# Performance work log

Hardware: AMD Instinct MI355X
Metric: run time of the kernel (lower is better)

The kernel has to match this reference:

```python
import jax, jax.numpy as jnp
import numpy as np

H = 128   # hidden_size
DYN = 2   # dynamic_features


def setup_inputs() -> dict:
    B, S, STAT = 256, 64, 2
    key = jax.random.key(0)
    ks = jax.random.split(key, 9)
    sc = 0.05
    return {
        "static": jax.random.normal(ks[0], (B, STAT, S), jnp.float32),
        "static_embeddings": jax.random.normal(ks[1], (B, H, S), jnp.float32),
        "dynamic": jax.random.uniform(ks[2], (B, DYN, S), jnp.float32),
        # dynamic_embedding: Conv1d(2 -> 128, k=1)
        "dyn_w": jax.random.normal(ks[3], (H, DYN), jnp.float32) * sc,
        "dyn_b": jnp.zeros((H,), jnp.float32),
        # decoder_input_dynamic_embedding: Conv1d(128 -> 128, k=1)
        "in_w": jax.random.normal(ks[4], (H, H), jnp.float32) * sc,
        "in_b": jnp.zeros((H,), jnp.float32),
        # GRU (single layer, batch_first), torch gate order r,z,n
        "w_ih": jax.random.normal(ks[5], (3 * H, H), jnp.float32) * sc,
        "w_hh": jax.random.normal(ks[6], (3 * H, H), jnp.float32) * sc,
        "b_ih": jnp.zeros((3 * H,), jnp.float32),
        "b_hh": jnp.zeros((3 * H,), jnp.float32),
        # DoubleAttention: scores = v . tanh(W [static; dynamic; hidden])
        "W_att": jax.random.normal(ks[7], (H, 3 * H), jnp.float32) * sc,
        "v_att": jax.random.normal(ks[8], (H,), jnp.float32) * sc,
    }


def _pointer_forward(static_embeddings, dynamic, dyn_w, dyn_b, in_w, in_b,
                     w_ih, w_hh, b_ih, b_hh, W_att, v_att):
    B, Hd, S = static_embeddings.shape
    NEG = jnp.asarray(-1e9, static_embeddings.dtype)
    base = jax.random.key(42)

    def gru_cell(x, h):  # torch nn.GRU single step
        gi = x @ w_ih.T + b_ih
        gh = h @ w_hh.T + b_hh
        ir, iz, i_n = jnp.split(gi, 3, axis=-1)
        hr, hz, h_n = jnp.split(gh, 3, axis=-1)
        r = jax.nn.sigmoid(ir + hr)
        z = jax.nn.sigmoid(iz + hz)
        n = jnp.tanh(i_n + r * h_n)
        return (1.0 - z) * n + z * h

    first_mask = jnp.zeros((B, S), static_embeddings.dtype).at[:, 0].set(1.0)

    def step(carry, i):
        dec_in, h, visited, dyn = carry
        # decoder_input_dynamic_embedding: 1x1 conv == per-token linear
        x = dec_in @ in_w.T + in_b                      # [B,H]
        h = gru_cell(x, h)                              # decoder_output == new hidden
        # i==0: only depot (index 0) is selectable; afterwards: unvisited nodes
        mask = jnp.where(i == 0, first_mask, 1.0 - visited)
        dyn_emb = jnp.einsum('bds,hd->bhs', dyn, dyn_w) + dyn_b[None, :, None]
        ctx = jnp.concatenate(
            [static_embeddings, dyn_emb,
             jnp.broadcast_to(h[:, :, None], (B, Hd, S))], axis=1)  # [B,3H,S]
        scores = jnp.einsum('h,bhs->bs', v_att,
                            jnp.tanh(jnp.einsum('hk,bks->bhs', W_att, ctx)))
        logits = jnp.where(mask > 0, scores, NEG)       # -inf on masked positions
        ptr = jax.random.categorical(jax.random.fold_in(base, i), logits)  # sample
        logp = jnp.take_along_axis(jax.nn.log_softmax(logits, -1),
                                   ptr[:, None], axis=1)[:, 0]
        sel = (jnp.arange(S)[None, :] == ptr[:, None]).astype(dyn.dtype)  # [B,S]
        visited = jnp.maximum(visited, sel)
        dyn = dyn * (1.0 - sel)[:, None, :]             # update_dynamic_state
        # original feeds the (conv-transformed) decoder input back to itself
        return (x, h, visited, dyn), (ptr, logp)

    init = (static_embeddings[:, :, 0],                  # decoder_input = emb of node 0
            jnp.zeros((B, Hd), static_embeddings.dtype),  # GRU hidden
            jnp.zeros((B, S), static_embeddings.dtype),   # visited
            dynamic)
    _, (tours, logps) = jax.lax.scan(step, init, jnp.arange(S))
    return tours.T, logps.T  # [B,S], [B,S]


def reference(static, static_embeddings, dynamic, dyn_w, dyn_b, in_w, in_b,
              w_ih, w_hh, b_ih, b_hh, W_att, v_att):
    # dropout layers are identity in eval mode; `static` is only used for logging
    return _pointer_forward(static_embeddings, dynamic, dyn_w, dyn_b, in_w, in_b,
                            w_ih, w_hh, b_ih, b_hh, W_att, v_att)
```

## Files before the change

kernel.cpp:

```cpp
#include <hip/hip_runtime.h>
#include <stdint.h>


#define BN 256
#define SN 64
#define HN 128
#define NEGV (-1.0e9f)
#define TINYF 1.17549435e-38f

#define OFF_A   0
#define OFF_GI  8192
#define OFF_WHC 8192
#define OFF_SET 16384
#define OFF_UT  24832
#define OFF_HC  33280
#define OFF_KK  33536
#define OFF_SV  33664
#define OFF_DY  33792
#define OFF_WD  33920
#define OFF_CV  34176
#define SMEM_FLOATS 34304

__device__ __forceinline__ uint32_t rotl32(uint32_t v, int d) {
  return (v << d) | (v >> (32 - d));
}

__device__ __forceinline__ void threefry2x32(uint32_t k0, uint32_t k1,
                                             uint32_t x0, uint32_t x1,
                                             uint32_t& o0, uint32_t& o1) {
  uint32_t ks2 = k0 ^ k1 ^ 0x1BD11BDAu;
  x0 += k0; x1 += k1;
  x0 += x1; x1 = rotl32(x1, 13); x1 ^= x0;
  x0 += x1; x1 = rotl32(x1, 15); x1 ^= x0;
  x0 += x1; x1 = rotl32(x1, 26); x1 ^= x0;
  x0 += x1; x1 = rotl32(x1, 6);  x1 ^= x0;
  x0 += k1; x1 += ks2 + 1u;
  x0 += x1; x1 = rotl32(x1, 17); x1 ^= x0;
  x0 += x1; x1 = rotl32(x1, 29); x1 ^= x0;
  x0 += x1; x1 = rotl32(x1, 16); x1 ^= x0;
  x0 += x1; x1 = rotl32(x1, 24); x1 ^= x0;
  x0 += ks2; x1 += k0 + 2u;
  x0 += x1; x1 = rotl32(x1, 13); x1 ^= x0;
  x0 += x1; x1 = rotl32(x1, 15); x1 ^= x0;
  x0 += x1; x1 = rotl32(x1, 26); x1 ^= x0;
  x0 += x1; x1 = rotl32(x1, 6);  x1 ^= x0;
  x0 += k0; x1 += k1 + 3u;
  x0 += x1; x1 = rotl32(x1, 17); x1 ^= x0;
  x0 += x1; x1 = rotl32(x1, 29); x1 ^= x0;
  x0 += x1; x1 = rotl32(x1, 16); x1 ^= x0;
  x0 += x1; x1 = rotl32(x1, 24); x1 ^= x0;
  x0 += k1; x1 += ks2 + 4u;
  x0 += x1; x1 = rotl32(x1, 13); x1 ^= x0;
  x0 += x1; x1 = rotl32(x1, 15); x1 ^= x0;
  x0 += x1; x1 = rotl32(x1, 26); x1 ^= x0;
  x0 += x1; x1 = rotl32(x1, 6);  x1 ^= x0;
  x0 += ks2; x1 += k0 + 5u;
  o0 = x0; o1 = x1;
}

__device__ __forceinline__ float jax_gumbel(uint32_t k0, uint32_t k1, int j) {
  uint32_t o0, o1;
  threefry2x32(k0, k1, 0u, (uint32_t)j, o0, o1);
  uint32_t bits = o0 ^ o1;
  uint32_t ub = (bits >> 9) | 0x3F800000u;
  float u = __uint_as_float(ub) - 1.0f;
  u = fmaxf(u + TINYF, TINYF);
  return -logf(-logf(u));
}

__device__ __forceinline__ float ftanh(float x) {
  float ax = fabsf(x);
  float e = __expf(-2.0f * ax);
  float r = (1.0f - e) * __builtin_amdgcn_rcpf(1.0f + e);
  return copysignf(r, x);
}

__device__ __forceinline__ float fsig(float x) {
  return __builtin_amdgcn_rcpf(1.0f + __expf(-x));
}

__global__ void k0_dyn(const float* __restrict__ W_att, const float* __restrict__ dyn_w,
                       const float* __restrict__ dyn_b, float* __restrict__ Wd,
                       float* __restrict__ cv) {
  int h = threadIdx.x;
  float w0 = 0.f, w1 = 0.f, cc = 0.f;
  for (int k = 0; k < HN; ++k) {
    float w = W_att[h * 384 + 128 + k];
    w0 = fmaf(w, dyn_w[2 * k + 0], w0);
    w1 = fmaf(w, dyn_w[2 * k + 1], w1);
    cc = fmaf(w, dyn_b[k], cc);
  }
  Wd[2 * h] = w0; Wd[2 * h + 1] = w1; cv[h] = cc;
}

__global__ __launch_bounds__(1024) void mega(
    const float* __restrict__ SE, const float* __restrict__ dynamic,
    const float* __restrict__ in_w, const float* __restrict__ in_b,
    const float* __restrict__ w_ih, const float* __restrict__ b_ih,
    const float* __restrict__ w_hh, const float* __restrict__ b_hh,
    const float* __restrict__ W_att, const float* __restrict__ v_att,
    const float* __restrict__ Wd, const float* __restrict__ cv,
    float* __restrict__ out) {
  extern __shared__ float sm[];
  int b = blockIdx.x, t = threadIdx.x;
  float* A   = sm + OFF_A;
  float* GIl = sm + OFF_GI;
  float* WHC = sm + OFF_WHC;
  float* SET = sm + OFF_SET;
  float* UT  = sm + OFF_UT;
  float* HC  = sm + OFF_HC;
  uint32_t* KK = (uint32_t*)(sm + OFF_KK);
  float* SV  = sm + OFF_SV;
  float* DY  = sm + OFF_DY;
  float* WDs = sm + OFF_WD;
  float* CVs = sm + OFF_CV;

  int ml = t >> 3, ks = t & 7;

  if (t < 64) {
    uint32_t o0, o1;
    threefry2x32(0u, 42u, 0u, (uint32_t)t, o0, o1);
    KK[2 * t] = o0; KK[2 * t + 1] = o1;
  }
  if (t < 128) {
    SV[t]  = v_att[t];
    DY[t]  = dynamic[b * 128 + t];
    CVs[t] = cv[t];
    HC[t]  = SE[b * 8192 + t * 64];
  }
  if (t < 256) WDs[t] = Wd[t];
  __syncthreads();

  {
    float4 wv[4];
#pragma unroll
    for (int q = 0; q < 4; ++q)
      wv[q] = *(const float4*)(in_w + ml * HN + q * 32 + ks * 4);
    float bib = in_b[ml];
    for (int ii = 0; ii < SN; ++ii) {
      const float* xc = HC + (ii & 1) * 128;
      float* xn = HC + ((ii + 1) & 1) * 128;
      float a0 = 0.f, a1 = 0.f, a2 = 0.f, a3 = 0.f;
#pragma unroll
      for (int q = 0; q < 4; ++q) {
        float4 x4 = *(const float4*)(xc + q * 32 + ks * 4);
        a0 = fmaf(wv[q].x, x4.x, a0);
        a1 = fmaf(wv[q].y, x4.y, a1);
        a2 = fmaf(wv[q].z, x4.z, a2);
        a3 = fmaf(wv[q].w, x4.w, a3);
      }
      float s = (a0 + a1) + (a2 + a3);
      s += __shfl_xor(s, 1); s += __shfl_xor(s, 2); s += __shfl_xor(s, 4);
      if (ks == 0) {
        float xv = s + bib;
        A[ii * 128 + ml] = xv;
        xn[ml] = xv;
      }
      __syncthreads();
    }
  }

  {
    float4 wv[3][4]; float bi[3];
#pragma unroll
    for (int j = 0; j < 3; ++j) {
#pragma unroll
      for (int q = 0; q < 4; ++q)
        wv[j][q] = *(const float4*)(w_ih + (ml + 128 * j) * HN + q * 32 + ks * 4);
      bi[j] = b_ih[ml + 128 * j];
    }
    for (int n = 0; n < SN; ++n) {
      float4 x4[4];
#pragma unroll
      for (int q = 0; q < 4; ++q)
        x4[q] = *(const float4*)(A + n * 128 + q * 32 + ks * 4);
      float sum[3];
#pragma unroll
      for (int j = 0; j < 3; ++j) {
        float a0 = 0.f, a1 = 0.f, a2 = 0.f, a3 = 0.f;
#pragma unroll
        for (int q = 0; q < 4; ++q) {
          a0 = fmaf(wv[j][q].x, x4[q].x, a0);
          a1 = fmaf(wv[j][q].y, x4[q].y, a1);
          a2 = fmaf(wv[j][q].z, x4[q].z, a2);
          a3 = fmaf(wv[j][q].w, x4[q].w, a3);
        }
        float s = (a0 + a1) + (a2 + a3);
        s += __shfl_xor(s, 1); s += __shfl_xor(s, 2); s += __shfl_xor(s, 4);
        sum[j] = s + bi[j];
      }
      if (ks == 0) {
#pragma unroll
        for (int j = 0; j < 3; ++j) GIl[n * 384 + ml + 128 * j] = sum[j];
      }
    }
    __syncthreads();
  }

  if (t < 256) HC[t] = 0.f;
  __syncthreads();
  {
    float4 wv[3][4]; float bh[3];
#pragma unroll
    for (int j = 0; j < 3; ++j) {
#pragma unroll
      for (int q = 0; q < 4; ++q)
        wv[j][q] = *(const float4*)(w_hh + (ml + 128 * j) * HN + q * 32 + ks * 4);
      bh[j] = b_hh[ml + 128 * j];
    }
    float hp = 0.f;
    for (int ii = 0; ii < SN; ++ii) {
      const float* hcr = HC + (ii & 1) * 128;
      float* hcw = HC + ((ii + 1) & 1) * 128;
      float4 x4[4];
#pragma unroll
      for (int q = 0; q < 4; ++q)
        x4[q] = *(const float4*)(hcr + q * 32 + ks * 4);
      float sum[3];
#pragma unroll
      for (int j = 0; j < 3; ++j) {
        float a0 = 0.f, a1 = 0.f, a2 = 0.f, a3 = 0.f;
#pragma unroll
        for (int q = 0; q < 4; ++q) {
          a0 = fmaf(wv[j][q].x, x4[q].x, a0);
          a1 = fmaf(wv[j][q].y, x4[q].y, a1);
          a2 = fmaf(wv[j][q].z, x4[q].z, a2);
          a3 = fmaf(wv[j][q].w, x4[q].w, a3);
        }
        float s = (a0 + a1) + (a2 + a3);
        s += __shfl_xor(s, 1); s += __shfl_xor(s, 2); s += __shfl_xor(s, 4);
        sum[j] = s + bh[j];
      }
      if (ks == 0) {
        const float* gr = GIl + ii * 384;
        float r = fsig(gr[ml] + sum[0]);
        float z = fsig(gr[128 + ml] + sum[1]);
        float nn = ftanh(gr[256 + ml] + r * sum[2]);
        float hn = (1.0f - z) * nn + z * hp;
        hcw[ml] = hn;
        A[ii * 128 + ml] = hn;
        hp = hn;
      }
      __syncthreads();
    }
  }

  {
    float4 wv[4];
#pragma unroll
    for (int q = 0; q < 4; ++q)
      wv[q] = *(const float4*)(W_att + ml * 384 + 256 + q * 32 + ks * 4);
    for (int n = 0; n < SN; ++n) {
      float a0 = 0.f, a1 = 0.f, a2 = 0.f, a3 = 0.f;
#pragma unroll
      for (int q = 0; q < 4; ++q) {
        float4 x4 = *(const float4*)(A + n * 128 + q * 32 + ks * 4);
        a0 = fmaf(wv[q].x, x4.x, a0);
        a1 = fmaf(wv[q].y, x4.y, a1);
        a2 = fmaf(wv[q].z, x4.z, a2);
        a3 = fmaf(wv[q].w, x4.w, a3);
      }
      float s = (a0 + a1) + (a2 + a3);
      s += __shfl_xor(s, 1); s += __shfl_xor(s, 2); s += __shfl_xor(s, 4);
      if (ks == 0) WHC[n * 128 + ml] = s;
    }
    __syncthreads();
  }

#pragma unroll
  for (int p = 0; p < 8; ++p) {
    int idx = p * 1024 + t;
    int h = idx >> 6, s = idx & 63;
    SET[s * 132 + h] = SE[b * 8192 + idx];
  }
  __syncthreads();

  {
    float4 wv[4];
#pragma unroll
    for (int q = 0; q < 4; ++q)
      wv[q] = *(const float4*)(W_att + ml * 384 + q * 32 + ks * 4);
    float wd0 = WDs[2 * ml], wd1 = WDs[2 * ml + 1], cvm = CVs[ml];
    for (int n = 0; n < SN; ++n) {
      float a0 = 0.f, a1 = 0.f, a2 = 0.f, a3 = 0.f;
#pragma unroll
      for (int q = 0; q < 4; ++q) {
        float4 x4 = *(const float4*)(SET + n * 132 + q * 32 + ks * 4);
        a0 = fmaf(wv[q].x, x4.x, a0);
        a1 = fmaf(wv[q].y, x4.y, a1);
        a2 = fmaf(wv[q].z, x4.z, a2);
        a3 = fmaf(wv[q].w, x4.w, a3);
      }
      float s = (a0 + a1) + (a2 + a3);
      s += __shfl_xor(s, 1); s += __shfl_xor(s, 2); s += __shfl_xor(s, 4);
      if (ks == 0) {
        float d0 = DY[n], d1 = DY[64 + n];
        UT[ml * 66 + n] = s + wd0 * d0 + wd1 * d1 + cvm;
      }
    }
    __syncthreads();
  }

  {
    int s = t & 63, w = t >> 6;
    float acc[4];
#pragma unroll
    for (int j = 0; j < 4; ++j) acc[j] = 0.f;
    for (int h = 0; h < HN; h += 4) {
      float u0 = UT[(h + 0) * 66 + s];
      float u1 = UT[(h + 1) * 66 + s];
      float u2 = UT[(h + 2) * 66 + s];
      float u3 = UT[(h + 3) * 66 + s];
      float4 v4 = *(const float4*)(SV + h);
#pragma unroll
      for (int j = 0; j < 4; ++j) {
        float4 wh = *(const float4*)(WHC + (w * 4 + j) * 128 + h);
        float a = acc[j];
        a = fmaf(v4.x, ftanh(u0 + wh.x), a);
        a = fmaf(v4.y, ftanh(u1 + wh.y), a);
        a = fmaf(v4.z, ftanh(u2 + wh.z), a);
        a = fmaf(v4.w, ftanh(u3 + wh.w), a);
        acc[j] = a;
      }
    }
    __syncthreads();
#pragma unroll
    for (int j = 0; j < 4; ++j) A[(w * 4 + j) * 64 + s] = acc[j];
    __syncthreads();
  }

  {
    float* G = A + 4096;
#pragma unroll
    for (int p = 0; p < 4; ++p) {
      int idx = p * 1024 + t;
      int i = idx >> 6;
      G[idx] = jax_gumbel(KK[2 * i], KK[2 * i + 1], b * 64 + (idx & 63));
    }
    __syncthreads();
  }

  if (t < 64) {
    const float* Pl = A;
    const float* Gl = A + 4096;
    int s = t;
    bool visited = false;
    for (int i = 0; i < SN; ++i) {
      float score = Pl[i * 64 + s];
      bool allowed = (i == 0) ? (s == 0) : (!visited);
      float logit = allowed ? score : NEGV;
      float z = logit + Gl[i * 64 + s];
      float bz = z; int bi = s;
#pragma unroll
      for (int off = 32; off > 0; off >>= 1) {
        float oz = __shfl_xor(bz, off);
        int oi = __shfl_xor(bi, off);
        if (oz > bz || (oz == bz && oi < bi)) { bz = oz; bi = oi; }
      }
      int ptr = bi;
      float m = logit;
#pragma unroll
      for (int off = 32; off > 0; off >>= 1) m = fmaxf(m, __shfl_xor(m, off));
      float e = expf(logit - m);
      float sum = e;
#pragma unroll
      for (int off = 32; off > 0; off >>= 1) sum += __shfl_xor(sum, off);
      float chosen = __shfl(logit, ptr);
      float logp = (chosen - m) - logf(sum);
      if (s == ptr) visited = true;
      if (s == 0) {
        out[b * SN + i] = (float)ptr;
        out[BN * SN + b * SN + i] = logp;
      }
    }
  }
}

extern "C" void kernel_launch(void* const* d_in, const int* in_sizes, int n_in,
                              void* d_out, int out_size, void* d_ws, size_t ws_size,
                              hipStream_t stream) {
  const float* SE    = (const float*)d_in[1];
  const float* dynam = (const float*)d_in[2];
  const float* dyn_w = (const float*)d_in[3];
  const float* dyn_b = (const float*)d_in[4];
  const float* in_w  = (const float*)d_in[5];
  const float* in_b  = (const float*)d_in[6];
  const float* w_ih  = (const float*)d_in[7];
  const float* w_hh  = (const float*)d_in[8];
  const float* b_ih  = (const float*)d_in[9];
  const float* b_hh  = (const float*)d_in[10];
  const float* W_att = (const float*)d_in[11];
  const float* v_att = (const float*)d_in[12];
  float* out = (float*)d_out;
  float* ws = (float*)d_ws;

  float* Wd = ws;
  float* cv = ws + 256;

  (void)hipFuncSetAttribute((const void*)mega,
                            hipFuncAttributeMaxDynamicSharedMemorySize,
                            SMEM_FLOATS * 4);

  hipLaunchKernelGGL(k0_dyn, dim3(1), dim3(128), 0, stream,
                     W_att, dyn_w, dyn_b, Wd, cv);
  hipLaunchKernelGGL(mega, dim3(BN), dim3(1024), SMEM_FLOATS * 4, stream,
                     SE, dynam, in_w, in_b, w_ih, b_ih, w_hh, b_hh,
                     W_att, v_att, Wd, cv, out);
}
```

Measured before the change: 347.3 us.

## Split mega kernel into recurrence and attention kernels with 512-thread blocks

The single 1024-thread-per-batch kernel becomes two 512-thread kernels. The first runs the input-embedding recurrence, the register-blocked GI projection (written to global scratch) and the GRU recurrence, with w_hh split between LDS and registers and GI prefetched two steps ahead. The second does the attention projections, scoring, Gumbel sampling and pointer selection, reading hidden states back from global memory. Threefry key generation moves to the setup kernel. The change aims to cut per-step sync cost in the sequential recurrences and raise occupancy, at the price of extra global traffic and a second launch.

```diff
diff --git a/kernel.cpp b/kernel.cpp
--- a/kernel.cpp
+++ b/kernel.cpp
@@ -7,19 +7,6 @@
 #define HN 128
 #define NEGV (-1.0e9f)
 #define TINYF 1.17549435e-38f
-
-#define OFF_A   0
-#define OFF_GI  8192
-#define OFF_WHC 8192
-#define OFF_SET 16384
-#define OFF_UT  24832
-#define OFF_HC  33280
-#define OFF_KK  33536
-#define OFF_SV  33664
-#define OFF_DY  33792
-#define OFF_WD  33920
-#define OFF_CV  34176
-#define SMEM_FLOATS 34304
 
 __device__ __forceinline__ uint32_t rotl32(uint32_t v, int d) {
   return (v << d) | (v >> (32 - d));
@@ -81,8 +68,13 @@
 
 __global__ void k0_dyn(const float* __restrict__ W_att, const float* __restrict__ dyn_w,
                        const float* __restrict__ dyn_b, float* __restrict__ Wd,
-                       float* __restrict__ cv) {
+                       float* __restrict__ cv, uint32_t* __restrict__ keys) {
   int h = threadIdx.x;
+  if (h < 64) {
+    uint32_t o0, o1;
+    threefry2x32(0u, 42u, 0u, (uint32_t)h, o0, o1);
+    keys[2 * h] = o0; keys[2 * h + 1] = o1;
+  }
   float w0 = 0.f, w1 = 0.f, cc = 0.f;
   for (int k = 0; k < HN; ++k) {
     float w = W_att[h * 384 + 128 + k];
@@ -93,64 +85,49 @@
   Wd[2 * h] = w0; Wd[2 * h + 1] = w1; cv[h] = cc;
 }
 
-__global__ __launch_bounds__(1024) void mega(
-    const float* __restrict__ SE, const float* __restrict__ dynamic,
+#define AB_A   0
+#define AB_WL  8192
+#define AB_HC  34304
+#define AB_GSH 34560
+#define AB_SMEM (34944 * 4)
+
+__global__ __launch_bounds__(512) void kAB(
+    const float* __restrict__ SE,
     const float* __restrict__ in_w, const float* __restrict__ in_b,
     const float* __restrict__ w_ih, const float* __restrict__ b_ih,
     const float* __restrict__ w_hh, const float* __restrict__ b_hh,
-    const float* __restrict__ W_att, const float* __restrict__ v_att,
-    const float* __restrict__ Wd, const float* __restrict__ cv,
-    float* __restrict__ out) {
+    float* __restrict__ GI_g, float* __restrict__ H_g) {
   extern __shared__ float sm[];
+  float* A   = sm + AB_A;
+  float* WL  = sm + AB_WL;
+  float* HC  = sm + AB_HC;
+  float* GSH = sm + AB_GSH;
   int b = blockIdx.x, t = threadIdx.x;
-  float* A   = sm + OFF_A;
-  float* GIl = sm + OFF_GI;
-  float* WHC = sm + OFF_WHC;
-  float* SET = sm + OFF_SET;
-  float* UT  = sm + OFF_UT;
-  float* HC  = sm + OFF_HC;
-  uint32_t* KK = (uint32_t*)(sm + OFF_KK);
-  float* SV  = sm + OFF_SV;
-  float* DY  = sm + OFF_DY;
-  float* WDs = sm + OFF_WD;
-  float* CVs = sm + OFF_CV;
-
-  int ml = t >> 3, ks = t & 7;
-
-  if (t < 64) {
-    uint32_t o0, o1;
-    threefry2x32(0u, 42u, 0u, (uint32_t)t, o0, o1);
-    KK[2 * t] = o0; KK[2 * t + 1] = o1;
-  }
-  if (t < 128) {
-    SV[t]  = v_att[t];
-    DY[t]  = dynamic[b * 128 + t];
-    CVs[t] = cv[t];
-    HC[t]  = SE[b * 8192 + t * 64];
-  }
-  if (t < 256) WDs[t] = Wd[t];
+
+  if (t < 128) HC[t] = SE[b * 8192 + t * 64];
   __syncthreads();
 
   {
-    float4 wv[4];
-#pragma unroll
-    for (int q = 0; q < 4; ++q)
-      wv[q] = *(const float4*)(in_w + ml * HN + q * 32 + ks * 4);
+    int ml = t >> 2, ks = t & 3;
+    float4 wv[8];
+#pragma unroll
+    for (int q = 0; q < 8; ++q)
+      wv[q] = *(const float4*)(in_w + ml * HN + q * 16 + ks * 4);
     float bib = in_b[ml];
     for (int ii = 0; ii < SN; ++ii) {
       const float* xc = HC + (ii & 1) * 128;
       float* xn = HC + ((ii + 1) & 1) * 128;
       float a0 = 0.f, a1 = 0.f, a2 = 0.f, a3 = 0.f;
 #pragma unroll
-      for (int q = 0; q < 4; ++q) {
-        float4 x4 = *(const float4*)(xc + q * 32 + ks * 4);
+      for (int q = 0; q < 8; ++q) {
+        float4 x4 = *(const float4*)(xc + q * 16 + ks * 4);
         a0 = fmaf(wv[q].x, x4.x, a0);
         a1 = fmaf(wv[q].y, x4.y, a1);
         a2 = fmaf(wv[q].z, x4.z, a2);
         a3 = fmaf(wv[q].w, x4.w, a3);
       }
       float s = (a0 + a1) + (a2 + a3);
-      s += __shfl_xor(s, 1); s += __shfl_xor(s, 2); s += __shfl_xor(s, 4);
+      s += __shfl_xor(s, 1); s += __shfl_xor(s, 2);
       if (ks == 0) {
         float xv = s + bib;
         A[ii * 128 + ml] = xv;
@@ -160,141 +137,198 @@
     }
   }
 
-  {
-    float4 wv[3][4]; float bi[3];
-#pragma unroll
-    for (int j = 0; j < 3; ++j) {
-#pragma unroll
-      for (int q = 0; q < 4; ++q)
-        wv[j][q] = *(const float4*)(w_ih + (ml + 128 * j) * HN + q * 32 + ks * 4);
-      bi[j] = b_ih[ml + 128 * j];
-    }
-    for (int n = 0; n < SN; ++n) {
-      float4 x4[4];
-#pragma unroll
-      for (int q = 0; q < 4; ++q)
-        x4[q] = *(const float4*)(A + n * 128 + q * 32 + ks * 4);
-      float sum[3];
-#pragma unroll
-      for (int j = 0; j < 3; ++j) {
-        float a0 = 0.f, a1 = 0.f, a2 = 0.f, a3 = 0.f;
-#pragma unroll
-        for (int q = 0; q < 4; ++q) {
-          a0 = fmaf(wv[j][q].x, x4[q].x, a0);
-          a1 = fmaf(wv[j][q].y, x4[q].y, a1);
-          a2 = fmaf(wv[j][q].z, x4[q].z, a2);
-          a3 = fmaf(wv[j][q].w, x4[q].w, a3);
+  for (int idx = t; idx < 24576; idx += 512) {
+    int m = idx >> 6, k = idx & 63;
+    WL[m * 68 + k] = w_hh[m * 128 + k];
+  }
+
+  {
+    int ml = t >> 2, ks = t & 3;
+    float bi[3];
+#pragma unroll
+    for (int j = 0; j < 3; ++j) bi[j] = b_ih[ml + 128 * j];
+    for (int g = 0; g < 8; ++g) {
+      float acc[3][8];
+#pragma unroll
+      for (int j = 0; j < 3; ++j)
+#pragma unroll
+        for (int nn = 0; nn < 8; ++nn) acc[j][nn] = 0.f;
+#pragma unroll
+      for (int p = 0; p < 4; ++p) {
+        float4 wv[3][2];
+#pragma unroll
+        for (int j = 0; j < 3; ++j) {
+          wv[j][0] = *(const float4*)(w_ih + (ml + 128 * j) * HN + p * 32 + ks * 4);
+          wv[j][1] = *(const float4*)(w_ih + (ml + 128 * j) * HN + p * 32 + 16 + ks * 4);
         }
-        float s = (a0 + a1) + (a2 + a3);
-        s += __shfl_xor(s, 1); s += __shfl_xor(s, 2); s += __shfl_xor(s, 4);
-        sum[j] = s + bi[j];
-      }
-      if (ks == 0) {
-#pragma unroll
-        for (int j = 0; j < 3; ++j) GIl[n * 384 + ml + 128 * j] = sum[j];
-      }
-    }
-    __syncthreads();
-  }
-
+#pragma unroll
+        for (int nn = 0; nn < 8; ++nn) {
+          int n = g * 8 + nn;
+          float4 x0 = *(const float4*)(A + n * 128 + p * 32 + ks * 4);
+          float4 x1 = *(const float4*)(A + n * 128 + p * 32 + 16 + ks * 4);
+#pragma unroll
+          for (int j = 0; j < 3; ++j) {
+            float a = acc[j][nn];
+            a = fmaf(wv[j][0].x, x0.x, a);
+            a = fmaf(wv[j][0].y, x0.y, a);
+            a = fmaf(wv[j][0].z, x0.z, a);
+            a = fmaf(wv[j][0].w, x0.w, a);
+            a = fmaf(wv[j][1].x, x1.x, a);
+            a = fmaf(wv[j][1].y, x1.y, a);
+            a = fmaf(wv[j][1].z, x1.z, a);
+            a = fmaf(wv[j][1].w, x1.w, a);
+            acc[j][nn] = a;
+          }
+        }
+      }
+#pragma unroll
+      for (int j = 0; j < 3; ++j)
+#pragma unroll
+        for (int nn = 0; nn < 8; ++nn) {
+          float s = acc[j][nn];
+          s += __shfl_xor(s, 1); s += __shfl_xor(s, 2);
+          if (ks == 0)
+            GI_g[b * 24576 + (g * 8 + nn) * 384 + ml + 128 * j] = s + bi[j];
+        }
+    }
+  }
+  __threadfence();
   if (t < 256) HC[t] = 0.f;
   __syncthreads();
-  {
-    float4 wv[3][4]; float bh[3];
+
+  {
+    int ml = t >> 2, ks = t & 3;
+    const float4* WL4 = (const float4*)WL;
+    float4 wu[3][4]; float bh[3];
 #pragma unroll
     for (int j = 0; j < 3; ++j) {
 #pragma unroll
       for (int q = 0; q < 4; ++q)
-        wv[j][q] = *(const float4*)(w_hh + (ml + 128 * j) * HN + q * 32 + ks * 4);
+        wu[j][q] = *(const float4*)(w_hh + (ml + 128 * j) * HN + 64 + q * 16 + ks * 4);
       bh[j] = b_hh[ml + 128 * j];
+    }
+    float gv0 = 0.f, gv1 = 0.f;
+    if (t < 384) {
+      gv0 = GI_g[b * 24576 + 0 * 384 + t];
+      gv1 = GI_g[b * 24576 + 1 * 384 + t];
     }
     float hp = 0.f;
     for (int ii = 0; ii < SN; ++ii) {
       const float* hcr = HC + (ii & 1) * 128;
       float* hcw = HC + ((ii + 1) & 1) * 128;
-      float4 x4[4];
-#pragma unroll
-      for (int q = 0; q < 4; ++q)
-        x4[q] = *(const float4*)(hcr + q * 32 + ks * 4);
-      float sum[3];
-#pragma unroll
-      for (int j = 0; j < 3; ++j) {
-        float a0 = 0.f, a1 = 0.f, a2 = 0.f, a3 = 0.f;
-#pragma unroll
-        for (int q = 0; q < 4; ++q) {
-          a0 = fmaf(wv[j][q].x, x4[q].x, a0);
-          a1 = fmaf(wv[j][q].y, x4[q].y, a1);
-          a2 = fmaf(wv[j][q].z, x4[q].z, a2);
-          a3 = fmaf(wv[j][q].w, x4[q].w, a3);
-        }
-        float s = (a0 + a1) + (a2 + a3);
-        s += __shfl_xor(s, 1); s += __shfl_xor(s, 2); s += __shfl_xor(s, 4);
-        sum[j] = s + bh[j];
-      }
+      float s0 = 0.f, s1 = 0.f, s2 = 0.f;
+#pragma unroll
+      for (int q = 0; q < 4; ++q) {
+        float4 xl = *(const float4*)(hcr + q * 16 + ks * 4);
+        float4 xu = *(const float4*)(hcr + 64 + q * 16 + ks * 4);
+        float4 w0 = WL4[(ml) * 17 + q * 4 + ks];
+        float4 w1 = WL4[(ml + 128) * 17 + q * 4 + ks];
+        float4 w2 = WL4[(ml + 256) * 17 + q * 4 + ks];
+        s0 = fmaf(w0.x, xl.x, s0); s0 = fmaf(w0.y, xl.y, s0);
+        s0 = fmaf(w0.z, xl.z, s0); s0 = fmaf(w0.w, xl.w, s0);
+        s1 = fmaf(w1.x, xl.x, s1); s1 = fmaf(w1.y, xl.y, s1);
+        s1 = fmaf(w1.z, xl.z, s1); s1 = fmaf(w1.w, xl.w, s1);
+        s2 = fmaf(w2.x, xl.x, s2); s2 = fmaf(w2.y, xl.y, s2);
+        s2 = fmaf(w2.z, xl.z, s2); s2 = fmaf(w2.w, xl.w, s2);
+        s0 = fmaf(wu[0][q].x, xu.x, s0); s0 = fmaf(wu[0][q].y, xu.y, s0);
+        s0 = fmaf(wu[0][q].z, xu.z, s0); s0 = fmaf(wu[0][q].w, xu.w, s0);
+        s1 = fmaf(wu[1][q].x, xu.x, s1); s1 = fmaf(wu[1][q].y, xu.y, s1);
+        s1 = fmaf(wu[1][q].z, xu.z, s1); s1 = fmaf(wu[1][q].w, xu.w, s1);
+        s2 = fmaf(wu[2][q].x, xu.x, s2); s2 = fmaf(wu[2][q].y, xu.y, s2);
+        s2 = fmaf(wu[2][q].z, xu.z, s2); s2 = fmaf(wu[2][q].w, xu.w, s2);
+      }
+      s0 += __shfl_xor(s0, 1); s0 += __shfl_xor(s0, 2);
+      s1 += __shfl_xor(s1, 1); s1 += __shfl_xor(s1, 2);
+      s2 += __shfl_xor(s2, 1); s2 += __shfl_xor(s2, 2);
+      if (t < 384) GSH[t] = gv0;
+      gv0 = gv1;
+      gv1 = (ii + 2 < SN && t < 384) ? GI_g[b * 24576 + (ii + 2) * 384 + t] : 0.f;
+      __syncthreads();
       if (ks == 0) {
-        const float* gr = GIl + ii * 384;
-        float r = fsig(gr[ml] + sum[0]);
-        float z = fsig(gr[128 + ml] + sum[1]);
-        float nn = ftanh(gr[256 + ml] + r * sum[2]);
+        float r = fsig(GSH[ml] + s0 + bh[0]);
+        float z = fsig(GSH[128 + ml] + s1 + bh[1]);
+        float nn = ftanh(GSH[256 + ml] + r * (s2 + bh[2]));
         float hn = (1.0f - z) * nn + z * hp;
         hcw[ml] = hn;
-        A[ii * 128 + ml] = hn;
+        H_g[(b * SN + ii) * HN + ml] = hn;
         hp = hn;
       }
       __syncthreads();
     }
   }
-
-  {
-    float4 wv[4];
-#pragma unroll
-    for (int q = 0; q < 4; ++q)
-      wv[q] = *(const float4*)(W_att + ml * 384 + 256 + q * 32 + ks * 4);
+}
+
+#define BC_H   0
+#define BC_SET 8192
+#define BC_WHC 16640
+#define BC_UT  24832
+#define BC_SMEM (33280 * 4)
+
+__global__ __launch_bounds__(512) void kBCD(
+    const float* __restrict__ SE, const float* __restrict__ dynamic,
+    const float* __restrict__ W_att, const float* __restrict__ v_att,
+    const float* __restrict__ Wd, const float* __restrict__ cv,
+    const uint32_t* __restrict__ keys,
+    const float* __restrict__ H_g, float* __restrict__ out) {
+  extern __shared__ float sm[];
+  float* Hl  = sm + BC_H;
+  float* SET = sm + BC_SET;
+  float* WHC = sm + BC_WHC;
+  float* UT  = sm + BC_UT;
+  int b = blockIdx.x, t = threadIdx.x;
+#pragma unroll
+  for (int p = 0; p < 4; ++p)
+    ((float4*)Hl)[p * 512 + t] = ((const float4*)(H_g + b * 8192))[p * 512 + t];
+  for (int p = 0; p < 16; ++p) {
+    int idx = p * 512 + t;
+    int h = idx >> 6, s = idx & 63;
+    SET[s * 132 + h] = SE[b * 8192 + idx];
+  }
+  __syncthreads();
+
+  {
+    int ml = t >> 2, ks = t & 3;
+    float4 wv[8];
+#pragma unroll
+    for (int q = 0; q < 8; ++q)
+      wv[q] = *(const float4*)(W_att + ml * 384 + 256 + q * 16 + ks * 4);
     for (int n = 0; n < SN; ++n) {
       float a0 = 0.f, a1 = 0.f, a2 = 0.f, a3 = 0.f;
 #pragma unroll
-      for (int q = 0; q < 4; ++q) {
-        float4 x4 = *(const float4*)(A + n * 128 + q * 32 + ks * 4);
+      for (int q = 0; q < 8; ++q) {
+        float4 x4 = *(const float4*)(Hl + n * 128 + q * 16 + ks * 4);
         a0 = fmaf(wv[q].x, x4.x, a0);
         a1 = fmaf(wv[q].y, x4.y, a1);
         a2 = fmaf(wv[q].z, x4.z, a2);
         a3 = fmaf(wv[q].w, x4.w, a3);
       }
       float s = (a0 + a1) + (a2 + a3);
-      s += __shfl_xor(s, 1); s += __shfl_xor(s, 2); s += __shfl_xor(s, 4);
+      s += __shfl_xor(s, 1); s += __shfl_xor(s, 2);
       if (ks == 0) WHC[n * 128 + ml] = s;
     }
-    __syncthreads();
-  }
-
-#pragma unroll
-  for (int p = 0; p < 8; ++p) {
-    int idx = p * 1024 + t;
-    int h = idx >> 6, s = idx & 63;
-    SET[s * 132 + h] = SE[b * 8192 + idx];
-  }
-  __syncthreads();
-
-  {
-    float4 wv[4];
-#pragma unroll
-    for (int q = 0; q < 4; ++q)
-      wv[q] = *(const float4*)(W_att + ml * 384 + q * 32 + ks * 4);
-    float wd0 = WDs[2 * ml], wd1 = WDs[2 * ml + 1], cvm = CVs[ml];
+  }
+
+  {
+    int ml = t >> 2, ks = t & 3;
+    float4 wv[8];
+#pragma unroll
+    for (int q = 0; q < 8; ++q)
+      wv[q] = *(const float4*)(W_att + ml * 384 + q * 16 + ks * 4);
+    float wd0 = Wd[2 * ml], wd1 = Wd[2 * ml + 1], cvm = cv[ml];
     for (int n = 0; n < SN; ++n) {
       float a0 = 0.f, a1 = 0.f, a2 = 0.f, a3 = 0.f;
 #pragma unroll
-      for (int q = 0; q < 4; ++q) {
-        float4 x4 = *(const float4*)(SET + n * 132 + q * 32 + ks * 4);
+      for (int q = 0; q < 8; ++q) {
+        float4 x4 = *(const float4*)(SET + n * 132 + q * 16 + ks * 4);
         a0 = fmaf(wv[q].x, x4.x, a0);
         a1 = fmaf(wv[q].y, x4.y, a1);
         a2 = fmaf(wv[q].z, x4.z, a2);
         a3 = fmaf(wv[q].w, x4.w, a3);
       }
       float s = (a0 + a1) + (a2 + a3);
-      s += __shfl_xor(s, 1); s += __shfl_xor(s, 2); s += __shfl_xor(s, 4);
+      s += __shfl_xor(s, 1); s += __shfl_xor(s, 2);
       if (ks == 0) {
-        float d0 = DY[n], d1 = DY[64 + n];
+        float d0 = dynamic[b * 128 + n], d1 = dynamic[b * 128 + 64 + n];
         UT[ml * 66 + n] = s + wd0 * d0 + wd1 * d1 + cvm;
       }
     }
@@ -303,18 +337,18 @@
 
   {
     int s = t & 63, w = t >> 6;
-    float acc[4];
-#pragma unroll
-    for (int j = 0; j < 4; ++j) acc[j] = 0.f;
+    float acc[8];
+#pragma unroll
+    for (int j = 0; j < 8; ++j) acc[j] = 0.f;
     for (int h = 0; h < HN; h += 4) {
       float u0 = UT[(h + 0) * 66 + s];
       float u1 = UT[(h + 1) * 66 + s];
       float u2 = UT[(h + 2) * 66 + s];
       float u3 = UT[(h + 3) * 66 + s];
-      float4 v4 = *(const float4*)(SV + h);
-#pragma unroll
-      for (int j = 0; j < 4; ++j) {
-        float4 wh = *(const float4*)(WHC + (w * 4 + j) * 128 + h);
+      float4 v4 = *(const float4*)(v_att + h);
+#pragma unroll
+      for (int j = 0; j < 8; ++j) {
+        float4 wh = *(const float4*)(WHC + (w * 8 + j) * 128 + h);
         float a = acc[j];
         a = fmaf(v4.x, ftanh(u0 + wh.x), a);
         a = fmaf(v4.y, ftanh(u1 + wh.y), a);
@@ -325,24 +359,22 @@
     }
     __syncthreads();
 #pragma unroll
-    for (int j = 0; j < 4; ++j) A[(w * 4 + j) * 64 + s] = acc[j];
+    for (int j = 0; j < 8; ++j) sm[(w * 8 + j) * 64 + s] = acc[j];
+  }
+
+  {
+    float* G = sm + 4096;
+    for (int p = 0; p < 8; ++p) {
+      int idx = p * 512 + t;
+      int i = idx >> 6;
+      G[idx] = jax_gumbel(keys[2 * i], keys[2 * i + 1], b * 64 + (idx & 63));
+    }
     __syncthreads();
   }
 
-  {
-    float* G = A + 4096;
-#pragma unroll
-    for (int p = 0; p < 4; ++p) {
-      int idx = p * 1024 + t;
-      int i = idx >> 6;
-      G[idx] = jax_gumbel(KK[2 * i], KK[2 * i + 1], b * 64 + (idx & 63));
-    }
-    __syncthreads();
-  }
-
   if (t < 64) {
-    const float* Pl = A;
-    const float* Gl = A + 4096;
+    const float* Pl = sm;
+    const float* Gl = sm + 4096;
     int s = t;
     bool visited = false;
     for (int i = 0; i < SN; ++i) {
@@ -394,16 +426,21 @@
   float* out = (float*)d_out;
   float* ws = (float*)d_ws;
 
-  float* Wd = ws;
-  float* cv = ws + 256;
-
-  (void)hipFuncSetAttribute((const void*)mega,
-                            hipFuncAttributeMaxDynamicSharedMemorySize,
-                            SMEM_FLOATS * 4);
+  float* GI_g = ws;
+  float* H_g  = ws + 6291456;
+  float* Wd   = ws + 8388608;
+  float* cv   = Wd + 256;
+  uint32_t* keys = (uint32_t*)(cv + 128);
+
+  (void)hipFuncSetAttribute((const void*)kAB,
+                            hipFuncAttributeMaxDynamicSharedMemorySize, AB_SMEM);
+  (void)hipFuncSetAttribute((const void*)kBCD,
+                            hipFuncAttributeMaxDynamicSharedMemorySize, BC_SMEM);
 
   hipLaunchKernelGGL(k0_dyn, dim3(1), dim3(128), 0, stream,
-                     W_att, dyn_w, dyn_b, Wd, cv);
-  hipLaunchKernelGGL(mega, dim3(BN), dim3(1024), SMEM_FLOATS * 4, stream,
-                     SE, dynam, in_w, in_b, w_ih, b_ih, w_hh, b_hh,
-                     W_att, v_att, Wd, cv, out);
-}
+                     W_att, dyn_w, dyn_b, Wd, cv, keys);
+  hipLaunchKernelGGL(kAB, dim3(BN), dim3(512), AB_SMEM, stream,
+                     SE, in_w, in_b, w_ih, b_ih, w_hh, b_hh, GI_g, H_g);
+  hipLaunchKernelGGL(kBCD, dim3(BN), dim3(512), BC_SMEM, stream,
+                     SE, dynam, W_att, v_att, Wd, cv, keys, H_g, out);
+}
```

After: 733.1 us. 111% more time.
